# Performance work log

Hardware: AMD Instinct MI355X
Metric: run time of the kernel (lower is better)

## Reference

```python
import jax, jax.numpy as jnp
import numpy as np
import math

B, N, F_DIM = 8, 256, 768
K = 128          # num_kernel / num_rbf
H = 32           # num_heads (rpe_heads, shared)
EMBED = 768      # embed_dim
N_LAYERS = 12
CUT_LO, CUT_HI = 0.0, 5.0
ALPHA = 5.0 / (CUT_HI - CUT_LO)


def setup_inputs() -> dict:
    key = jax.random.key(0)
    ks = jax.random.split(key, 8)
    node_features = jax.random.normal(ks[0], (B, N, F_DIM), dtype=jnp.float32)
    pos = jax.random.normal(ks[1], (B, N, 3), dtype=jnp.float32)
    # ExponentialLayer params
    start = math.exp(-CUT_HI + CUT_LO)
    means = jnp.linspace(start, 1.0, K, dtype=jnp.float32)
    betas = jnp.full((K,), (2.0 / K * (1.0 - start)) ** -2, dtype=jnp.float32)
    # NonLinear(K -> K -> H), torch init: normal(0, 0.02/sqrt(n_layers)), bias 0
    std = 0.02 / math.sqrt(N_LAYERS)
    w1 = jax.random.normal(ks[2], (K, K), dtype=jnp.float32) * std
    b1 = jnp.zeros((K,), dtype=jnp.float32)
    w2 = jax.random.normal(ks[3], (K, H), dtype=jnp.float32) * std
    b2 = jnp.zeros((H,), dtype=jnp.float32)
    # edge_proj Linear(K -> EMBED)
    ew = jax.random.normal(ks[4], (K, EMBED), dtype=jnp.float32) * std
    eb = jnp.zeros((EMBED,), dtype=jnp.float32)
    return {"node_features": node_features, "pos": pos, "means": means,
            "betas": betas, "w1": w1, "b1": b1, "w2": w2, "b2": b2,
            "ew": ew, "eb": eb}


def reference(node_features, pos, means, betas, w1, b1, w2, b2, ew, eb):
    # padding mask: nodes whose feature vector is all zeros -> [B, N]
    padding_mask = jnp.all(node_features == 0, axis=-1)
    # pairwise deltas and distances
    delta_pos = pos[:, :, None, :] - pos[:, None, :, :]          # [B,N,N,3]
    radial = jnp.sum(delta_pos ** 2, axis=-1)                    # [B,N,N]
    pos_mask = radial > 0
    # safe sqrt (equivalent to sqrt + nan_to_num; grad-safe at 0)
    dist = jnp.sqrt(jnp.where(pos_mask, radial, 1.0)) * pos_mask
    # ExponentialLayer RBF expansion -> [B,N,N,K]
    d = dist[..., None]
    edge_feature = jnp.exp(-betas * (jnp.exp(ALPHA * (-d + CUT_LO)) - means) ** 2)
    # NonLinear: Linear -> exact GELU -> Linear
    hidden = jax.nn.gelu(edge_feature @ w1 + b1, approximate=False)
    bias_heads = hidden @ w2 + b2                                # [B,N,N,H]
    # permute to [B,H,N,N] and mask padded key nodes with -1e20
    graph_attn_bias = jnp.transpose(bias_heads, (0, 3, 1, 2))
    graph_attn_bias = jnp.where(padding_mask[:, None, None, :], -1e20,
                                graph_attn_bias)
    # zero edge features whose second node is padded, then reduce over it
    ef = jnp.where(padding_mask[:, None, :, None], 0.0, edge_feature)
    sum_edge_features = jnp.sum(ef, axis=-2)                     # [B,N,K]
    merge_edge_features = sum_edge_features @ ew + eb            # [B,N,EMBED]
    return graph_attn_bias, merge_edge_features, delta_pos
```

## Files before the change

### kernel.cpp

```cpp
#include <hip/hip_runtime.h>
#include <math.h>

typedef float f32x4 __attribute__((ext_vector_type(4)));

#define RBF_START 0.006737946999085467f
#define RBF_H     (0.993262053000915f / 127.0f)
#define RBF_INVH  (127.0f / 0.993262053000915f)
#define RBF_BETA  (1.0f / ((2.0f/128.0f*0.993262053000915f) * (2.0f/128.0f*0.993262053000915f)))
#define KN 256

__global__ __launch_bounds__(256) void prep_kernel(
    const float* __restrict__ nf, int* __restrict__ mask,
    const float* __restrict__ w1, const float* __restrict__ b1,
    const float* __restrict__ w2, const float* __restrict__ b2,
    float* __restrict__ tableG) {
  int g = blockIdx.x, t = threadIdx.x;
  if (g < 2048) {
    const float* p = nf + (size_t)g * 768;
    bool nz = (p[t] != 0.f) || (p[t + 256] != 0.f) || (p[t + 512] != 0.f);
    __shared__ int wany[4];
    unsigned long long bal = __ballot(nz);
    if ((t & 63) == 0) wany[t >> 6] = (bal != 0ull);
    __syncthreads();
    if (t == 0) mask[g] = (wany[0] | wany[1] | wany[2] | wany[3]) ? 0 : 1;
  } else {
    int knot = g - 2048;
    float e = (float)knot * (1.0f / (float)KN);
    __shared__ float ef_s[128];
    __shared__ float hid_s[128];
    if (t < 128) {
      float mu = fmaf((float)t, RBF_H, RBF_START);
      float diff = e - mu;
      ef_s[t] = __expf(-RBF_BETA * diff * diff);
    }
    __syncthreads();
    if (t < 128) {
      float s = b1[t];
      for (int k = 0; k < 128; k++) s = fmaf(ef_s[k], w1[k * 128 + t], s);
      hid_s[t] = 0.5f * s * (1.0f + erff(s * 0.70710678118654752f));
    }
    __syncthreads();
    int h = t >> 3, seg = t & 7;
    float s = 0.f;
    const float* hp = hid_s + seg * 16;
    const float* wp = w2 + (seg * 16) * 32 + h;
#pragma unroll
    for (int m = 0; m < 16; m++) s = fmaf(hp[m], wp[m * 32], s);
    s += __shfl_xor(s, 1);
    s += __shfl_xor(s, 2);
    s += __shfl_xor(s, 4);
    if (seg == 0) tableG[h * (KN + 1) + knot] = s + b2[h];
  }
}

__global__ __launch_bounds__(256, 4) void main_kernel(
    const float* __restrict__ pos, const int* __restrict__ mask,
    const float* __restrict__ tableG,
    float* __restrict__ out0, float* __restrict__ out2,
    float* __restrict__ part) {
  __shared__ float T_s[32 * (KN + 1)];
  __shared__ float part_s[128];

  int t = threadIdx.x, g = blockIdx.x;
  int b = g >> 8, i = g & 255;

  {
    const f32x4* src = (const f32x4*)tableG;
    f32x4* dst = (f32x4*)T_s;
#pragma unroll
    for (int r = 0; r < 8; r++) dst[r * 256 + t] = src[r * 256 + t];
    if (t < 8) dst[2048 + t] = src[2048 + t];
  }
  if (t < 128) part_s[t] = 0.f;
  __syncthreads();

  int j = t;
  const float* pb = pos + b * 768;
  float pix = pb[i * 3 + 0], piy = pb[i * 3 + 1], piz = pb[i * 3 + 2];
  float dx = pix - pb[j * 3 + 0];
  float dy = piy - pb[j * 3 + 1];
  float dz = piz - pb[j * 3 + 2];
  float r2 = dx * dx + dy * dy + dz * dz;
  float d = (r2 > 0.f) ? sqrtf(r2) : 0.f;
  float e = __expf(-d);
  size_t base2 = ((size_t)g * 256 + (size_t)j) * 3;
  out2[base2 + 0] = dx; out2[base2 + 1] = dy; out2[base2 + 2] = dz;

  bool pad = mask[b * 256 + j] != 0;

  if (!pad) {
    int kc = (int)rintf((e - RBF_START) * RBF_INVH);
    kc = min(max(kc, 0), 127);
    int kb = kc - 8;
#pragma unroll
    for (int o = 0; o < 16; o++) {
      int k = kb + o;
      if (k >= 0 && k < 128) {
        float mu = fmaf((float)k, RBF_H, RBF_START);
        float diff = e - mu;
        atomicAdd(&part_s[k], __expf(-RBF_BETA * diff * diff));
      }
    }
  }

  size_t ob = (size_t)b * 2097152 + (size_t)i * 256 + (size_t)j;
  if (pad) {
#pragma unroll
    for (int h = 0; h < 32; h++) out0[ob + (size_t)h * 65536] = -1e20f;
  } else {
    float u = e * (float)KN;
    int i0 = (int)u; i0 = min(i0, KN - 1);
    float fr = u - (float)i0;
#pragma unroll
    for (int h = 0; h < 32; h++) {
      float lo = T_s[h * (KN + 1) + i0];
      float hi = T_s[h * (KN + 1) + i0 + 1];
      out0[ob + (size_t)h * 65536] = fmaf(fr, hi - lo, lo);
    }
  }

  __syncthreads();
  if (t < 128) part[(size_t)g * 128 + t] = part_s[t];
}

__global__ __launch_bounds__(256) void merge_kernel(const float* __restrict__ part,
                                                    const float* __restrict__ ew,
                                                    const float* __restrict__ eb,
                                                    float* __restrict__ out1) {
  __shared__ float s_s[8][128];
  int t = threadIdx.x;
  int r0 = blockIdx.x * 8;
  for (int idx = t; idx < 1024; idx += 256) {
    int row = idx >> 7, k = idx & 127;
    s_s[row][k] = part[(size_t)(r0 + row) * 128 + k];
  }
  __syncthreads();
  float acc[3][8];
#pragma unroll
  for (int c = 0; c < 3; c++)
#pragma unroll
    for (int r = 0; r < 8; r++) acc[c][r] = 0.f;
  for (int k = 0; k < 128; k++) {
    float w0 = ew[k * 768 + t];
    float w1v = ew[k * 768 + t + 256];
    float w2v = ew[k * 768 + t + 512];
#pragma unroll
    for (int r = 0; r < 8; r++) {
      float s = s_s[r][k];
      acc[0][r] += s * w0;
      acc[1][r] += s * w1v;
      acc[2][r] += s * w2v;
    }
  }
#pragma unroll
  for (int c = 0; c < 3; c++) {
    float ebv = eb[c * 256 + t];
#pragma unroll
    for (int r = 0; r < 8; r++)
      out1[(size_t)(r0 + r) * 768 + c * 256 + t] = acc[c][r] + ebv;
  }
}

extern "C" void kernel_launch(void* const* d_in, const int* in_sizes, int n_in,
                              void* d_out, int out_size, void* d_ws, size_t ws_size,
                              hipStream_t stream) {
    const float* nf    = (const float*)d_in[0];
    const float* pos   = (const float*)d_in[1];
    const float* w1    = (const float*)d_in[4];
    const float* b1    = (const float*)d_in[5];
    const float* w2    = (const float*)d_in[6];
    const float* b2    = (const float*)d_in[7];
    const float* ew    = (const float*)d_in[8];
    const float* eb    = (const float*)d_in[9];

    float* out0 = (float*)d_out;
    float* out1 = out0 + (size_t)8 * 32 * 256 * 256;
    float* out2 = out1 + (size_t)8 * 256 * 768;

    char* ws = (char*)d_ws;
    int*    mask   = (int*)ws;
    float*  tableG = (float*)(ws + 8192);
    float*  part   = (float*)(ws + 49152);

    hipLaunchKernelGGL(prep_kernel,  dim3(2305), dim3(256), 0, stream,
                       nf, mask, w1, b1, w2, b2, tableG);
    hipLaunchKernelGGL(main_kernel,  dim3(2048), dim3(256), 0, stream,
                       pos, mask, tableG, out0, out2, part);
    hipLaunchKernelGGL(merge_kernel, dim3(256),  dim3(256), 0, stream, part, ew, eb, out1);
}
```

Measured before the change: 168.5 us.

## Split bias output into per-head kernel with small per-head LUT and vector stores

The fused main kernel is split in two. An e-kernel computes distances, stores exp(-d) in a workspace buffer and does the RBF partial sums. A new bias kernel assigns one head per block, so it only stages that head's 256-entry interpolation table (as lo/hi pairs) in shared memory instead of the full 32-head table. It then writes the bias with 16-byte nontemporal stores. This cuts the per-block LDS load and occupancy pressure, and the output writes become vectorised. The cost is an extra 2 MB workspace round-trip for e and one more kernel launch.

```diff
diff --git a/kernel.cpp b/kernel.cpp
--- a/kernel.cpp
+++ b/kernel.cpp
@@ -2,6 +2,8 @@
 #include <math.h>
 
 typedef float f32x4 __attribute__((ext_vector_type(4)));
+typedef float f32x2 __attribute__((ext_vector_type(2)));
+typedef int   i32x4 __attribute__((ext_vector_type(4)));
 
 #define RBF_START 0.006737946999085467f
 #define RBF_H     (0.993262053000915f / 127.0f)
@@ -53,24 +55,12 @@
   }
 }
 
-__global__ __launch_bounds__(256, 4) void main_kernel(
+__global__ __launch_bounds__(256) void e_kernel(
     const float* __restrict__ pos, const int* __restrict__ mask,
-    const float* __restrict__ tableG,
-    float* __restrict__ out0, float* __restrict__ out2,
-    float* __restrict__ part) {
-  __shared__ float T_s[32 * (KN + 1)];
+    float* __restrict__ ebuf, float* __restrict__ out2, float* __restrict__ part) {
   __shared__ float part_s[128];
-
   int t = threadIdx.x, g = blockIdx.x;
   int b = g >> 8, i = g & 255;
-
-  {
-    const f32x4* src = (const f32x4*)tableG;
-    f32x4* dst = (f32x4*)T_s;
-#pragma unroll
-    for (int r = 0; r < 8; r++) dst[r * 256 + t] = src[r * 256 + t];
-    if (t < 8) dst[2048 + t] = src[2048 + t];
-  }
   if (t < 128) part_s[t] = 0.f;
   __syncthreads();
 
@@ -85,9 +75,9 @@
   float e = __expf(-d);
   size_t base2 = ((size_t)g * 256 + (size_t)j) * 3;
   out2[base2 + 0] = dx; out2[base2 + 1] = dy; out2[base2 + 2] = dz;
+  ebuf[(size_t)g * 256 + j] = e;
 
   bool pad = mask[b * 256 + j] != 0;
-
   if (!pad) {
     int kc = (int)rintf((e - RBF_START) * RBF_INVH);
     kc = min(max(kc, 0), 127);
@@ -102,25 +92,45 @@
       }
     }
   }
-
-  size_t ob = (size_t)b * 2097152 + (size_t)i * 256 + (size_t)j;
-  if (pad) {
-#pragma unroll
-    for (int h = 0; h < 32; h++) out0[ob + (size_t)h * 65536] = -1e20f;
-  } else {
-    float u = e * (float)KN;
-    int i0 = (int)u; i0 = min(i0, KN - 1);
-    float fr = u - (float)i0;
-#pragma unroll
-    for (int h = 0; h < 32; h++) {
-      float lo = T_s[h * (KN + 1) + i0];
-      float hi = T_s[h * (KN + 1) + i0 + 1];
-      out0[ob + (size_t)h * 65536] = fmaf(fr, hi - lo, lo);
-    }
-  }
-
   __syncthreads();
   if (t < 128) part[(size_t)g * 128 + t] = part_s[t];
+}
+
+__global__ __launch_bounds__(256, 4) void bias_kernel(
+    const float* __restrict__ tableG, const int* __restrict__ mask,
+    const float* __restrict__ ebuf, float* __restrict__ out0) {
+  __shared__ f32x2 Tp[256];
+
+  int t = threadIdx.x, bid = blockIdx.x;
+  int b = bid >> 7, h = (bid >> 2) & 31, qi = bid & 3;
+
+  {
+    float lo = tableG[h * (KN + 1) + t];
+    float hi = tableG[h * (KN + 1) + t + 1];
+    Tp[t] = (f32x2){lo, hi};
+  }
+  int w = t >> 6, l = t & 63;
+  i32x4 m4 = *(const i32x4*)&mask[b * 256 + l * 4];
+  __syncthreads();
+
+  size_t ebase = ((size_t)(b * 256 + qi * 64 + w)) * 256 + (size_t)(l * 4);
+  size_t obase = ((size_t)((b * 32 + h) * 256 + qi * 64 + w)) * 256 + (size_t)(l * 4);
+
+#pragma unroll 4
+  for (int ii = 0; ii < 16; ii++) {
+    f32x4 e4 = *(const f32x4*)&ebuf[ebase + (size_t)ii * 1024];
+    f32x4 o;
+#pragma unroll
+    for (int r = 0; r < 4; r++) {
+      float u = e4[r] * (float)KN;
+      int i0 = (int)u; i0 = min(i0, KN - 1);
+      float fr = u - (float)i0;
+      f32x2 tp = Tp[i0];
+      float v = fmaf(fr, tp[1] - tp[0], tp[0]);
+      o[r] = m4[r] ? -1e20f : v;
+    }
+    __builtin_nontemporal_store(o, (f32x4*)&out0[obase + (size_t)ii * 1024]);
+  }
 }
 
 __global__ __launch_bounds__(256) void merge_kernel(const float* __restrict__ part,
@@ -181,10 +191,13 @@
     int*    mask   = (int*)ws;
     float*  tableG = (float*)(ws + 8192);
     float*  part   = (float*)(ws + 49152);
-
-    hipLaunchKernelGGL(prep_kernel,  dim3(2305), dim3(256), 0, stream,
+    float*  ebuf   = (float*)(ws + 49152 + 1048576);
+
+    hipLaunchKernelGGL(prep_kernel, dim3(2305), dim3(256), 0, stream,
                        nf, mask, w1, b1, w2, b2, tableG);
-    hipLaunchKernelGGL(main_kernel,  dim3(2048), dim3(256), 0, stream,
-                       pos, mask, tableG, out0, out2, part);
-    hipLaunchKernelGGL(merge_kernel, dim3(256),  dim3(256), 0, stream, part, ew, eb, out1);
-}
+    hipLaunchKernelGGL(e_kernel,    dim3(2048), dim3(256), 0, stream,
+                       pos, mask, ebuf, out2, part);
+    hipLaunchKernelGGL(bias_kernel, dim3(1024), dim3(256), 0, stream,
+                       tableG, mask, ebuf, out0);
+    hipLaunchKernelGGL(merge_kernel, dim3(256), dim3(256), 0, stream, part, ew, eb, out1);
+}
```

Result: slower. 181.3 us (+7.6%).
